# Kernel tuning notes

Hardware: AMD Instinct MI355X
Metric: run time of the kernel (lower is better)

The kernel has to match this reference:

```python
import math
import jax, jax.numpy as jnp
import numpy as np

N_HEAD = 16

def skew(QEr):
    # QEr: (B, H, L, L) where last dim indexes relative positions via Er_t
    B, H, L, _ = QEr.shape
    padded = jnp.pad(QEr, ((0, 0), (0, 0), (0, 0), (1, 0)))        # (B,H,L,L+1)
    reshaped = padded.reshape(B, H, L + 1, L)                       # (B,H,L+1,L)
    return reshaped[:, :, 1:, :]                                    # (B,H,L,L)

def setup_inputs() -> dict:
    key = jax.random.key(0)
    ks = jax.random.split(key, 6)
    B, L, D = 2, 2048, 1024
    hs = D // N_HEAD
    block_size = 2048
    return {
        "x": jax.random.normal(ks[0], (B, L, D), dtype=jnp.float32),
        "W_attn": jax.random.normal(ks[1], (D, 3 * D), dtype=jnp.float32) * 0.02,
        "b_attn": jnp.zeros((3 * D,), dtype=jnp.float32),
        "W_proj": jax.random.normal(ks[2], (D, D), dtype=jnp.float32) * 0.02,
        "b_proj": jnp.zeros((D,), dtype=jnp.float32),
        "Er": jax.random.normal(ks[3], (block_size, hs), dtype=jnp.float32),
    }

def reference(x, W_attn, b_attn, W_proj, b_proj, Er):
    B, L, D = x.shape
    H = N_HEAD
    hs = D // H
    qkv = x @ W_attn + b_attn                                       # (B,L,3D)
    q, k, v = jnp.split(qkv, 3, axis=-1)
    q = q.reshape(B, L, H, hs).transpose(0, 2, 1, 3)                # (B,H,L,hs)
    k = k.reshape(B, L, H, hs).transpose(0, 2, 1, 3)
    v = v.reshape(B, L, H, hs).transpose(0, 2, 1, 3)
    start = Er.shape[0] - L
    Er_t = Er[start:, :].T                                          # (hs,L)
    QEr = jnp.einsum('bhld,de->bhle', q, Er_t)                      # (B,H,L,L)
    Srel = skew(QEr)
    QK_t = jnp.einsum('bhqd,bhkd->bhqk', q, k)
    scale = 1.0 / math.sqrt(hs)
    att = (QK_t + Srel) * scale
    causal = jnp.tril(jnp.ones((L, L), dtype=bool))
    att = jnp.where(causal[None, None, :, :], att, -jnp.inf)
    att = jax.nn.softmax(att, axis=-1)
    y = jnp.einsum('bhqk,bhkd->bhqd', att, v)                       # (B,H,L,hs)
    y = y.transpose(0, 2, 1, 3).reshape(B, L, D)
    return y @ W_proj + b_proj
```

## Files before the change

### kernel.cpp

```cpp
#include <hip/hip_runtime.h>
#include <stdint.h>

#define L_SEQ 2048
#define D_MODEL 1024
#define NHEAD 16
#define HS 64
#define B_BATCH 2
#define QSCALE 0.1803368801111243f

typedef __bf16 bf16x8 __attribute__((ext_vector_type(8)));
typedef float f32x4 __attribute__((ext_vector_type(4)));

__device__ __forceinline__ float fexp2(float x) {
  return __builtin_amdgcn_exp2f(x);
}

__device__ __forceinline__ unsigned short f2b(float f) {
  unsigned int u = __float_as_uint(f);
  u += 0x7fffu + ((u >> 16) & 1u);
  return (unsigned short)(u >> 16);
}
__device__ __forceinline__ float b2f(unsigned short s) {
  return __uint_as_float(((unsigned int)s) << 16);
}
__device__ __forceinline__ unsigned int pk2(float a, float b) {
  return (unsigned int)f2b(a) | ((unsigned int)f2b(b) << 16);
}

union U8 { uint4 v; unsigned short s[8]; };

__device__ __forceinline__ void ldsload16(const unsigned short* g, unsigned short* l) {
  __builtin_amdgcn_global_load_lds(
      (const __attribute__((address_space(1))) unsigned int*)g,
      (__attribute__((address_space(3))) unsigned int*)l, 16, 0, 0);
}

__device__ __forceinline__ bf16x8 frag_ld(const unsigned short* base, int row, int ks, int quad) {
  const int unit = (ks * 4 + quad) ^ (row & 7);
  return *(const bf16x8*)(base + row * 64 + unit * 8);
}
__device__ __forceinline__ bf16x8 frag_ld88(const unsigned short* base, int row, int ks, int quad) {
  const int unit = (ks * 4 + quad) ^ (row & 7);
  return *(const bf16x8*)(base + row * 88 + unit * 8);
}

__global__ __launch_bounds__(256) void prep(
    const float* __restrict__ x, const float* __restrict__ Wa,
    const float* __restrict__ Wp, const float* __restrict__ Er,
    unsigned short* __restrict__ xb, unsigned short* __restrict__ wabT,
    unsigned short* __restrict__ wpbT, unsigned short* __restrict__ erb) {
  __shared__ unsigned short tt[64][65];
  int gb = blockIdx.x;
  if (gb < 2048) {
    int i = gb * 256 + threadIdx.x;
    const float4* s4 = (const float4*)x;
    float4 a = s4[i * 2], b = s4[i * 2 + 1];
    U8 u;
    u.s[0] = f2b(a.x); u.s[1] = f2b(a.y); u.s[2] = f2b(a.z); u.s[3] = f2b(a.w);
    u.s[4] = f2b(b.x); u.s[5] = f2b(b.y); u.s[6] = f2b(b.z); u.s[7] = f2b(b.w);
    ((uint4*)xb)[i] = u.v;
    return;
  }
  gb -= 2048;
  if (gb < 66) {
    int i = gb * 256 + threadIdx.x;
    if (i < 16384) {
      const float4* s4 = (const float4*)Er;
      float4 a = s4[i * 2], b = s4[i * 2 + 1];
      U8 u;
      u.s[0] = f2b(a.x); u.s[1] = f2b(a.y); u.s[2] = f2b(a.z); u.s[3] = f2b(a.w);
      u.s[4] = f2b(b.x); u.s[5] = f2b(b.y); u.s[6] = f2b(b.z); u.s[7] = f2b(b.w);
      ((uint4*)erb)[i] = u.v;
    } else {
      ((uint4*)erb)[i] = make_uint4(0u, 0u, 0u, 0u);
    }
    return;
  }
  gb -= 66;
  const float* src;
  unsigned short* dst;
  int N, nbx;
  if (gb < 768) { src = Wa; dst = wabT; N = 3072; nbx = 48; }
  else { gb -= 768; src = Wp; dst = wpbT; N = 1024; nbx = 16; }
  const int n0 = (gb % nbx) * 64, k0 = (gb / nbx) * 64;
  const int c = threadIdx.x & 63, r0 = threadIdx.x >> 6;
#pragma unroll
  for (int i = 0; i < 16; i++) {
    int r = r0 * 16 + i;
    tt[r][c] = f2b(src[(size_t)(k0 + r) * N + n0 + c]);
  }
  __syncthreads();
  const int n = threadIdx.x >> 2, ks = (threadIdx.x & 3) * 16;
  U8 u0, u1;
#pragma unroll
  for (int j = 0; j < 8; j++) {
    u0.s[j] = tt[ks + j][n];
    u1.s[j] = tt[ks + 8 + j][n];
  }
  unsigned short* d = dst + (size_t)(n0 + n) * 1024 + k0 + ks;
  *(uint4*)d = u0.v;
  *(uint4*)(d + 8) = u1.v;
}

__global__ __launch_bounds__(256, 3) void gemm_qkv(
    const unsigned short* __restrict__ A, const unsigned short* __restrict__ Bt,
    const float* __restrict__ bias, unsigned short* __restrict__ qbuf,
    unsigned short* __restrict__ kbuf, unsigned short* __restrict__ vbufT,
    int M, int N, int K) {
  __shared__ unsigned short SMEM[2 * 128 * 64];
  unsigned short* As = SMEM;
  unsigned short* Bs = SMEM + 128 * 64;
  const int tid = threadIdx.x, lane = tid & 63, w = tid >> 6;
  const int wm = w >> 1, wn = w & 1, quad = lane >> 4, lc = lane & 15;
  const int bm = blockIdx.y, bn = blockIdx.x;
  const int l8 = lane >> 3, u8 = ((lane & 7) ^ l8) * 8;
  const unsigned short* Ab = A + (size_t)bm * 128 * K;
  const unsigned short* Bb = Bt + (size_t)bn * 128 * K;

  f32x4 z4 = {0.f, 0.f, 0.f, 0.f};
  f32x4 acc[4][4];
#pragma unroll
  for (int mb = 0; mb < 4; mb++)
#pragma unroll
    for (int nb = 0; nb < 4; nb++) acc[mb][nb] = z4;

  for (int kk = 0; kk < K; kk += 64) {
    if (kk) __syncthreads();
#pragma unroll
    for (int i = 0; i < 4; i++) {
      int ch = w * 4 + i;
      ldsload16(Ab + (size_t)(ch * 8 + l8) * K + kk + u8, &As[ch * 512]);
      ldsload16(Bb + (size_t)(ch * 8 + l8) * K + kk + u8, &Bs[ch * 512]);
    }
    __syncthreads();
#pragma unroll
    for (int ks = 0; ks < 2; ks++) {
      bf16x8 af[4], bfv[4];
#pragma unroll
      for (int mb = 0; mb < 4; mb++) af[mb] = frag_ld(As, wm * 64 + mb * 16 + lc, ks, quad);
#pragma unroll
      for (int nb = 0; nb < 4; nb++) bfv[nb] = frag_ld(Bs, wn * 64 + nb * 16 + lc, ks, quad);
#pragma unroll
      for (int mb = 0; mb < 4; mb++)
#pragma unroll
        for (int nb = 0; nb < 4; nb++)
          acc[mb][nb] = __builtin_amdgcn_mfma_f32_16x16x32_bf16(af[mb], bfv[nb],
                                                               acc[mb][nb], 0, 0, 0);
    }
  }

  if (bn < 16) {
#pragma unroll
    for (int nb = 0; nb < 4; nb++) {
      const int n = bn * 128 + wn * 64 + nb * 16 + lc;
      const float bv = bias[n];
      const int which = n >> 10;
      const int rem = n & 1023;
      const int h = rem >> 6, d = rem & 63;
      unsigned short* dst = which == 0 ? qbuf : kbuf;
      const float sc = which == 0 ? QSCALE : 1.0f;
#pragma unroll
      for (int mb = 0; mb < 4; mb++) {
#pragma unroll
        for (int reg = 0; reg < 4; reg++) {
          const int m = bm * 128 + wm * 64 + mb * 16 + quad * 4 + reg;
          const int b = m >> 11, l = m & 2047;
          float val = (acc[mb][nb][reg] + bv) * sc;
          dst[((size_t)(b * NHEAD + h) * L_SEQ + l) * HS + d] = f2b(val);
        }
      }
    }
  } else {
    __syncthreads();
    unsigned short* Vs = SMEM;
#pragma unroll
    for (int nb = 0; nb < 4; nb++) {
      const int n_loc = wn * 64 + nb * 16 + lc;
      const float bv = bias[bn * 128 + n_loc];
#pragma unroll
      for (int mb = 0; mb < 4; mb++) {
#pragma unroll
        for (int reg = 0; reg < 4; reg++) {
          const int m_loc = wm * 64 + mb * 16 + quad * 4 + reg;
          Vs[n_loc * 128 + (((m_loc >> 3) ^ (n_loc & 15)) << 3) + (m_loc & 7)] =
              f2b(acc[mb][nb][reg] + bv);
        }
      }
    }
    __syncthreads();
    const int n_loc = tid >> 1, mh = tid & 1;
    const int n_glob = bn * 128 + n_loc;
    const int rem = n_glob & 1023;
    const int h = rem >> 6, d = rem & 63;
    const int b = bm >> 4;
    unsigned short* dstb =
        vbufT + ((size_t)(b * NHEAD + h) * HS + d) * L_SEQ + (bm & 15) * 128;
#pragma unroll
    for (int c = 0; c < 8; c++) {
      const int cg = mh * 8 + c;
      const int u = cg ^ (n_loc & 15);
      *(uint4*)(dstb + cg * 8) = *(const uint4*)&Vs[n_loc * 128 + u * 8];
    }
  }
}

__global__ __launch_bounds__(256, 2) void gemm_proj(
    const unsigned short* __restrict__ A, const unsigned short* __restrict__ Bt,
    const float* __restrict__ bias, float* __restrict__ out, int M, int N, int K) {
  __shared__ unsigned short As[128 * 64];
  __shared__ unsigned short Bs[64 * 64];
  const int tid = threadIdx.x, lane = tid & 63, w = tid >> 6;
  const int quad = lane >> 4, lc = lane & 15;
  const int bm = blockIdx.y, bn = blockIdx.x;
  const int l8 = lane >> 3, u8 = ((lane & 7) ^ l8) * 8;
  const unsigned short* Ab = A + (size_t)bm * 128 * K;
  const unsigned short* Bb = Bt + (size_t)bn * 64 * K;

  f32x4 z4 = {0.f, 0.f, 0.f, 0.f};
  f32x4 acc[2][4];
#pragma unroll
  for (int mb = 0; mb < 2; mb++)
#pragma unroll
    for (int nb = 0; nb < 4; nb++) acc[mb][nb] = z4;

  for (int kk = 0; kk < K; kk += 64) {
    if (kk) __syncthreads();
#pragma unroll
    for (int i = 0; i < 4; i++) {
      int ch = w * 4 + i;
      ldsload16(Ab + (size_t)(ch * 8 + l8) * K + kk + u8, &As[ch * 512]);
    }
#pragma unroll
    for (int i = 0; i < 2; i++) {
      int ch = w * 2 + i;
      ldsload16(Bb + (size_t)(ch * 8 + l8) * K + kk + u8, &Bs[ch * 512]);
    }
    __syncthreads();
#pragma unroll
    for (int ks = 0; ks < 2; ks++) {
      bf16x8 af[2], bfv[4];
#pragma unroll
      for (int mb = 0; mb < 2; mb++) af[mb] = frag_ld(As, w * 32 + mb * 16 + lc, ks, quad);
#pragma unroll
      for (int nb = 0; nb < 4; nb++) bfv[nb] = frag_ld(Bs, nb * 16 + lc, ks, quad);
#pragma unroll
      for (int mb = 0; mb < 2; mb++)
#pragma unroll
        for (int nb = 0; nb < 4; nb++)
          acc[mb][nb] = __builtin_amdgcn_mfma_f32_16x16x32_bf16(af[mb], bfv[nb],
                                                               acc[mb][nb], 0, 0, 0);
    }
  }

#pragma unroll
  for (int nb = 0; nb < 4; nb++) {
    const int n = bn * 64 + nb * 16 + lc;
    const float bv = bias[n];
#pragma unroll
    for (int mb = 0; mb < 2; mb++) {
#pragma unroll
      for (int reg = 0; reg < 4; reg++) {
        const int m = bm * 128 + w * 32 + mb * 16 + quad * 4 + reg;
        out[(size_t)m * N + n] = acc[mb][nb][reg] + bv;
      }
    }
  }
}

__global__ __launch_bounds__(256, 2) void flash_attn_rel(
    const unsigned short* __restrict__ qb, const unsigned short* __restrict__ kb,
    const unsigned short* __restrict__ vbT, const unsigned short* __restrict__ erb,
    unsigned short* __restrict__ yb) {
  __shared__ unsigned short Ks[2][64 * 64];
  __shared__ unsigned short Vt[2][64 * 64];
  __shared__ unsigned short Es[2][128 * 64];
  __shared__ unsigned short TP[4 * 16 * 88];

  const int tid = threadIdx.x, lane = tid & 63, w = tid >> 6;
  const int quad = lane >> 4, lc = lane & 15;
  const int bh = blockIdx.x;
  const int b = bh >> 4, h = bh & 15;
  const int j = blockIdx.y;
  const int qts0 = 31 - j, qts1 = j;
  const size_t hoff = (size_t)bh * L_SEQ * HS;
  unsigned short* TPw = TP + w * (16 * 88);
  const int l8 = lane >> 3, u8 = ((lane & 7) ^ l8) * 8;
  const f32x4 z4 = {0.f, 0.f, 0.f, 0.f};
  const unsigned short* kgb = kb + hoff;
  const unsigned short* vgbT = vbT + hoff;
  const int ebw = 48 - w * 16;

  auto stage = [&](int q0s, int k0s, int bufi) {
#pragma unroll
    for (int i = 0; i < 2; i++) {
      int ch = w * 2 + i;
      ldsload16(kgb + (size_t)(k0s + ch * 8 + l8) * HS + u8, &Ks[bufi][ch * 512]);
      ldsload16(vgbT + (size_t)(ch * 8 + l8) * L_SEQ + k0s + u8, &Vt[bufi][ch * 512]);
    }
    const int e0 = (L_SEQ - 64) - q0s + k0s;
#pragma unroll
    for (int i = 0; i < 4; i++) {
      int ch = w * 4 + i;
      ldsload16(erb + (size_t)(e0 + ch * 8 + l8) * HS + u8, &Es[bufi][ch * 512]);
    }
  };

  int buf = 0;
  stage(qts0 * 64, 0, 0);

#pragma unroll 1
  for (int phase = 0; phase < 2; phase++) {
    const int q0 = (phase == 0 ? qts0 : qts1) * 64;
    const int qg0 = q0 + w * 16;

    bf16x8 qf[2];
    {
      const unsigned short* qrow = qb + hoff + (size_t)(qg0 + lc) * HS;
      qf[0] = *(const bf16x8*)(qrow + quad * 8);
      qf[1] = *(const bf16x8*)(qrow + 32 + quad * 8);
    }
    f32x4 Oacc[4];
#pragma unroll
    for (int db = 0; db < 4; db++) Oacc[db] = z4;
    float psum_acc = 0.0f;

#pragma unroll 1
    for (int k0 = 0; k0 <= q0; k0 += 64) {
      __syncthreads();
      if (k0 + 64 <= q0) stage(q0, k0 + 64, buf ^ 1);
      else if (phase == 0) stage(qts1 * 64, 0, buf ^ 1);

      const unsigned short* KsB = Ks[buf];
      const unsigned short* VtB = Vt[buf];
      const unsigned short* EsB = Es[buf];

      f32x4 sacc[4], tacc[5];
#pragma unroll
      for (int i = 0; i < 4; i++) sacc[i] = z4;
#pragma unroll
      for (int i = 0; i < 5; i++) tacc[i] = z4;
#pragma unroll
      for (int ks = 0; ks < 2; ks++) {
#pragma unroll
        for (int kbi = 0; kbi < 4; kbi++) {
          bf16x8 a = frag_ld(KsB, kbi * 16 + lc, ks, quad);
          sacc[kbi] = __builtin_amdgcn_mfma_f32_16x16x32_bf16(a, qf[ks], sacc[kbi], 0, 0, 0);
        }
#pragma unroll
        for (int eb = 0; eb < 5; eb++) {
          bf16x8 a = frag_ld(EsB, ebw + eb * 16 + lc, ks, quad);
          tacc[eb] = __builtin_amdgcn_mfma_f32_16x16x32_bf16(a, qf[ks], tacc[eb], 0, 0, 0);
        }
      }
#pragma unroll
      for (int eb = 0; eb < 5; eb++) {
        uint2 pk;
        pk.x = pk2(tacc[eb][0], tacc[eb][1]);
        pk.y = pk2(tacc[eb][2], tacc[eb][3]);
        *(uint2*)&TPw[lc * 88 + eb * 16 + quad * 4] = pk;
      }
      asm volatile("" ::: "memory");

      float p[4][4], ps = 0.0f;
      const int tbase = lc * 88 + (15 - lc);
      if (k0 == q0) {
        const int qrow = w * 16 + lc;
#pragma unroll
        for (int kbi = 0; kbi < 4; kbi++)
#pragma unroll
          for (int reg = 0; reg < 4; reg++) {
            const int kk = kbi * 16 + quad * 4 + reg;
            float t = b2f(TPw[tbase + kk]);
            float v = (kk > qrow) ? -1e30f : (sacc[kbi][reg] + t);
            p[kbi][reg] = fexp2(v);
            ps += p[kbi][reg];
          }
      } else {
#pragma unroll
        for (int kbi = 0; kbi < 4; kbi++)
#pragma unroll
          for (int reg = 0; reg < 4; reg++) {
            float t = b2f(TPw[tbase + kbi * 16 + quad * 4 + reg]);
            p[kbi][reg] = fexp2(sacc[kbi][reg] + t);
            ps += p[kbi][reg];
          }
      }
      psum_acc += ps;
#pragma unroll
      for (int kbi = 0; kbi < 4; kbi++) {
        uint2 pk;
        pk.x = pk2(p[kbi][0], p[kbi][1]);
        pk.y = pk2(p[kbi][2], p[kbi][3]);
        const int kk2 = kbi * 16 + quad * 4;
        *(uint2*)&TPw[lc * 88 + (((kk2 >> 3) ^ (lc & 7)) << 3) + (kk2 & 7)] = pk;
      }
      asm volatile("" ::: "memory");

#pragma unroll
      for (int ks = 0; ks < 2; ks++) {
        bf16x8 pf = frag_ld88(TPw, lc, ks, quad);
#pragma unroll
        for (int db = 0; db < 4; db++) {
          bf16x8 av = frag_ld(VtB, db * 16 + lc, ks, quad);
          Oacc[db] = __builtin_amdgcn_mfma_f32_16x16x32_bf16(av, pf, Oacc[db], 0, 0, 0);
        }
      }
      buf ^= 1;
    }

    psum_acc += __shfl_xor(psum_acc, 16, 64);
    psum_acc += __shfl_xor(psum_acc, 32, 64);
    const float inv = 1.0f / psum_acc;
    __syncthreads();
    unsigned short* Yt = TP;
#pragma unroll
    for (int db = 0; db < 4; db++) {
      uint2 pk;
      pk.x = pk2(Oacc[db][0] * inv, Oacc[db][1] * inv);
      pk.y = pk2(Oacc[db][2] * inv, Oacc[db][3] * inv);
      *(uint2*)&Yt[(w * 16 + lc) * 72 + db * 16 + quad * 4] = pk;
    }
    __syncthreads();
    {
      const int r = tid >> 2, seg = (tid & 3) * 16;
      uint4 a0 = *(const uint4*)&Yt[r * 72 + seg];
      uint4 a1 = *(const uint4*)&Yt[r * 72 + seg + 8];
      unsigned short* d = yb + (size_t)((size_t)b * L_SEQ + q0 + r) * D_MODEL + h * HS + seg;
      *(uint4*)d = a0;
      *(uint4*)(d + 8) = a1;
    }
  }
}

extern "C" void kernel_launch(void* const* d_in, const int* in_sizes, int n_in,
                              void* d_out, int out_size, void* d_ws, size_t ws_size,
                              hipStream_t stream) {
  const float* x = (const float*)d_in[0];
  const float* W_attn = (const float*)d_in[1];
  const float* b_attn = (const float*)d_in[2];
  const float* W_proj = (const float*)d_in[3];
  const float* b_proj = (const float*)d_in[4];
  const float* Er = (const float*)d_in[5];
  float* out = (float*)d_out;

  const int n_x = B_BATCH * L_SEQ * D_MODEL;
  const int n_wa = D_MODEL * 3 * D_MODEL;
  const int n_wp = D_MODEL * D_MODEL;
  const int n_er_pad = (L_SEQ + 64) * HS;
  const int n_head = B_BATCH * NHEAD * L_SEQ * HS;

  unsigned short* xb = (unsigned short*)d_ws;
  unsigned short* wabT = xb + n_x;
  unsigned short* wpbT = wabT + n_wa;
  unsigned short* erb = wpbT + n_wp;
  unsigned short* qbuf = erb + n_er_pad;
  unsigned short* kbuf = qbuf + n_head;
  unsigned short* vbufT = kbuf + n_head;
  unsigned short* ybuf = vbufT + n_head;

  prep<<<3138, 256, 0, stream>>>(x, W_attn, W_proj, Er, xb, wabT, wpbT, erb);

  gemm_qkv<<<dim3(24, 32), 256, 0, stream>>>(xb, wabT, b_attn, qbuf, kbuf, vbufT,
                                             B_BATCH * L_SEQ, 3 * D_MODEL, D_MODEL);

  flash_attn_rel<<<dim3(B_BATCH * NHEAD, 16), 256, 0, stream>>>(qbuf, kbuf, vbufT,
                                                                erb, ybuf);

  gemm_proj<<<dim3(16, 32), 256, 0, stream>>>(ybuf, wpbT, b_proj, out,
                                              B_BATCH * L_SEQ, D_MODEL, D_MODEL);
}
```

Measured before the change: 228.8 us.

## Process adjacent query tiles together to share K/V/Er tiles, drop double buffering

Each attention block now handles two adjacent 64-row query tiles at once instead of a mirrored pair processed one after the other. Each loaded K, V and a widened 192-row Er tile is reused by both tiles, which halves the K/V staging per unit of work. The LDS double buffering is removed and occupancy is raised to 3 blocks per SM. In exchange, global loads are no longer overlapped with compute, the load balance across blocks is worse than with the mirrored pairing, and the Er padding buffer grows to cover the extra rows.

```diff
diff --git a/kernel.cpp b/kernel.cpp
--- a/kernel.cpp
+++ b/kernel.cpp
@@ -62,7 +62,7 @@
     return;
   }
   gb -= 2048;
-  if (gb < 66) {
+  if (gb < 68) {
     int i = gb * 256 + threadIdx.x;
     if (i < 16384) {
       const float4* s4 = (const float4*)Er;
@@ -71,12 +71,12 @@
       u.s[0] = f2b(a.x); u.s[1] = f2b(a.y); u.s[2] = f2b(a.z); u.s[3] = f2b(a.w);
       u.s[4] = f2b(b.x); u.s[5] = f2b(b.y); u.s[6] = f2b(b.z); u.s[7] = f2b(b.w);
       ((uint4*)erb)[i] = u.v;
-    } else {
+    } else if (i < 17408) {
       ((uint4*)erb)[i] = make_uint4(0u, 0u, 0u, 0u);
     }
     return;
   }
-  gb -= 66;
+  gb -= 68;
   const float* src;
   unsigned short* dst;
   int N, nbx;
@@ -267,168 +267,192 @@
   }
 }
 
-__global__ __launch_bounds__(256, 2) void flash_attn_rel(
+__global__ __launch_bounds__(256, 3) void flash_attn_rel(
     const unsigned short* __restrict__ qb, const unsigned short* __restrict__ kb,
     const unsigned short* __restrict__ vbT, const unsigned short* __restrict__ erb,
     unsigned short* __restrict__ yb) {
-  __shared__ unsigned short Ks[2][64 * 64];
-  __shared__ unsigned short Vt[2][64 * 64];
-  __shared__ unsigned short Es[2][128 * 64];
+  __shared__ unsigned short Ks[64 * 64];
+  __shared__ unsigned short Vt[64 * 64];
+  __shared__ unsigned short Es[192 * 64];
   __shared__ unsigned short TP[4 * 16 * 88];
 
   const int tid = threadIdx.x, lane = tid & 63, w = tid >> 6;
   const int quad = lane >> 4, lc = lane & 15;
   const int bh = blockIdx.x;
   const int b = bh >> 4, h = bh & 15;
-  const int j = blockIdx.y;
-  const int qts0 = 31 - j, qts1 = j;
+  const int p = 15 - (int)blockIdx.y;
+  const int q0lo = 2 * p * 64, q0hi = q0lo + 64;
   const size_t hoff = (size_t)bh * L_SEQ * HS;
   unsigned short* TPw = TP + w * (16 * 88);
   const int l8 = lane >> 3, u8 = ((lane & 7) ^ l8) * 8;
   const f32x4 z4 = {0.f, 0.f, 0.f, 0.f};
   const unsigned short* kgb = kb + hoff;
   const unsigned short* vgbT = vbT + hoff;
-  const int ebw = 48 - w * 16;
-
-  auto stage = [&](int q0s, int k0s, int bufi) {
+
+  bf16x8 qfh[2], qfl[2];
+  {
+    const unsigned short* qh = qb + hoff + (size_t)(q0hi + w * 16 + lc) * HS;
+    const unsigned short* ql = qb + hoff + (size_t)(q0lo + w * 16 + lc) * HS;
+    qfh[0] = *(const bf16x8*)(qh + quad * 8);
+    qfh[1] = *(const bf16x8*)(qh + 32 + quad * 8);
+    qfl[0] = *(const bf16x8*)(ql + quad * 8);
+    qfl[1] = *(const bf16x8*)(ql + 32 + quad * 8);
+  }
+  f32x4 Oh[4], Ol[4];
+#pragma unroll
+  for (int db = 0; db < 4; db++) { Oh[db] = z4; Ol[db] = z4; }
+  float psh = 0.0f, psl = 0.0f;
+
+  auto softmax_pv = [&](f32x4 (&sacc)[4], f32x4 (&tacc)[5], bool diag,
+                        float& psum_acc, f32x4 (&Oacc)[4], bf16x8 (&vf)[2][4]) {
+#pragma unroll
+    for (int eb = 0; eb < 5; eb++) {
+      uint2 pk;
+      pk.x = pk2(tacc[eb][0], tacc[eb][1]);
+      pk.y = pk2(tacc[eb][2], tacc[eb][3]);
+      *(uint2*)&TPw[lc * 88 + eb * 16 + quad * 4] = pk;
+    }
+    asm volatile("" ::: "memory");
+    float pv[4][4], ps = 0.0f;
+    const int tbase = lc * 88 + (15 - lc);
+    if (diag) {
+      const int qrow = w * 16 + lc;
+#pragma unroll
+      for (int kbi = 0; kbi < 4; kbi++)
+#pragma unroll
+        for (int reg = 0; reg < 4; reg++) {
+          const int kk = kbi * 16 + quad * 4 + reg;
+          float t = b2f(TPw[tbase + kk]);
+          float v = (kk > qrow) ? -1e30f : (sacc[kbi][reg] + t);
+          pv[kbi][reg] = fexp2(v);
+          ps += pv[kbi][reg];
+        }
+    } else {
+#pragma unroll
+      for (int kbi = 0; kbi < 4; kbi++)
+#pragma unroll
+        for (int reg = 0; reg < 4; reg++) {
+          float t = b2f(TPw[tbase + kbi * 16 + quad * 4 + reg]);
+          pv[kbi][reg] = fexp2(sacc[kbi][reg] + t);
+          ps += pv[kbi][reg];
+        }
+    }
+    psum_acc += ps;
+#pragma unroll
+    for (int kbi = 0; kbi < 4; kbi++) {
+      uint2 pk;
+      pk.x = pk2(pv[kbi][0], pv[kbi][1]);
+      pk.y = pk2(pv[kbi][2], pv[kbi][3]);
+      const int kk2 = kbi * 16 + quad * 4;
+      *(uint2*)&TPw[lc * 88 + (((kk2 >> 3) ^ (lc & 7)) << 3) + (kk2 & 7)] = pk;
+    }
+    asm volatile("" ::: "memory");
+#pragma unroll
+    for (int ks = 0; ks < 2; ks++) {
+      bf16x8 pf = frag_ld88(TPw, lc, ks, quad);
+#pragma unroll
+      for (int db = 0; db < 4; db++)
+        Oacc[db] = __builtin_amdgcn_mfma_f32_16x16x32_bf16(vf[ks][db], pf, Oacc[db], 0, 0, 0);
+    }
+  };
+
+#pragma unroll 1
+  for (int k0 = 0; k0 <= q0hi; k0 += 64) {
+    const bool lo_active = (k0 <= q0lo);
+    __syncthreads();
 #pragma unroll
     for (int i = 0; i < 2; i++) {
       int ch = w * 2 + i;
-      ldsload16(kgb + (size_t)(k0s + ch * 8 + l8) * HS + u8, &Ks[bufi][ch * 512]);
-      ldsload16(vgbT + (size_t)(ch * 8 + l8) * L_SEQ + k0s + u8, &Vt[bufi][ch * 512]);
-    }
-    const int e0 = (L_SEQ - 64) - q0s + k0s;
-#pragma unroll
-    for (int i = 0; i < 4; i++) {
-      int ch = w * 4 + i;
-      ldsload16(erb + (size_t)(e0 + ch * 8 + l8) * HS + u8, &Es[bufi][ch * 512]);
-    }
-  };
-
-  int buf = 0;
-  stage(qts0 * 64, 0, 0);
-
+      ldsload16(kgb + (size_t)(k0 + ch * 8 + l8) * HS + u8, &Ks[ch * 512]);
+      ldsload16(vgbT + (size_t)(ch * 8 + l8) * L_SEQ + k0 + u8, &Vt[ch * 512]);
+    }
+    const int e0 = (L_SEQ - 64) - q0hi + k0;
+#pragma unroll
+    for (int i = 0; i < 6; i++) {
+      int ch = w * 6 + i;
+      ldsload16(erb + (size_t)(e0 + ch * 8 + l8) * HS + u8, &Es[ch * 512]);
+    }
+    __syncthreads();
+
+    f32x4 sh[4], sl[4];
+#pragma unroll
+    for (int i = 0; i < 4; i++) { sh[i] = z4; sl[i] = z4; }
+#pragma unroll
+    for (int ks = 0; ks < 2; ks++) {
+      bf16x8 kf[4];
+#pragma unroll
+      for (int kbi = 0; kbi < 4; kbi++) kf[kbi] = frag_ld(Ks, kbi * 16 + lc, ks, quad);
+#pragma unroll
+      for (int kbi = 0; kbi < 4; kbi++)
+        sh[kbi] = __builtin_amdgcn_mfma_f32_16x16x32_bf16(kf[kbi], qfh[ks], sh[kbi], 0, 0, 0);
+      if (lo_active) {
+#pragma unroll
+        for (int kbi = 0; kbi < 4; kbi++)
+          sl[kbi] = __builtin_amdgcn_mfma_f32_16x16x32_bf16(kf[kbi], qfl[ks], sl[kbi], 0, 0, 0);
+      }
+    }
+
+    f32x4 th[5];
+#pragma unroll
+    for (int i = 0; i < 5; i++) th[i] = z4;
+    const int rsh = 48 - w * 16;
+#pragma unroll
+    for (int ks = 0; ks < 2; ks++)
+#pragma unroll
+      for (int eb = 0; eb < 5; eb++)
+        th[eb] = __builtin_amdgcn_mfma_f32_16x16x32_bf16(
+            frag_ld(Es, rsh + eb * 16 + lc, ks, quad), qfh[ks], th[eb], 0, 0, 0);
+
+    bf16x8 vf[2][4];
+#pragma unroll
+    for (int ks = 0; ks < 2; ks++)
+#pragma unroll
+      for (int db = 0; db < 4; db++) vf[ks][db] = frag_ld(Vt, db * 16 + lc, ks, quad);
+
+    softmax_pv(sh, th, k0 == q0hi, psh, Oh, vf);
+
+    if (lo_active) {
+      f32x4 tl[5];
+#pragma unroll
+      for (int i = 0; i < 5; i++) tl[i] = z4;
+      const int rsl = 112 - w * 16;
+#pragma unroll
+      for (int ks = 0; ks < 2; ks++)
+#pragma unroll
+        for (int eb = 0; eb < 5; eb++)
+          tl[eb] = __builtin_amdgcn_mfma_f32_16x16x32_bf16(
+              frag_ld(Es, rsl + eb * 16 + lc, ks, quad), qfl[ks], tl[eb], 0, 0, 0);
+      softmax_pv(sl, tl, k0 == q0lo, psl, Ol, vf);
+    }
+  }
+
+  psh += __shfl_xor(psh, 16, 64);
+  psh += __shfl_xor(psh, 32, 64);
+  psl += __shfl_xor(psl, 16, 64);
+  psl += __shfl_xor(psl, 32, 64);
+  const float invh = 1.0f / psh, invl = 1.0f / psl;
+
+  unsigned short* Yt = TP;
 #pragma unroll 1
-  for (int phase = 0; phase < 2; phase++) {
-    const int q0 = (phase == 0 ? qts0 : qts1) * 64;
-    const int qg0 = q0 + w * 16;
-
-    bf16x8 qf[2];
-    {
-      const unsigned short* qrow = qb + hoff + (size_t)(qg0 + lc) * HS;
-      qf[0] = *(const bf16x8*)(qrow + quad * 8);
-      qf[1] = *(const bf16x8*)(qrow + 32 + quad * 8);
-    }
-    f32x4 Oacc[4];
-#pragma unroll
-    for (int db = 0; db < 4; db++) Oacc[db] = z4;
-    float psum_acc = 0.0f;
-
-#pragma unroll 1
-    for (int k0 = 0; k0 <= q0; k0 += 64) {
-      __syncthreads();
-      if (k0 + 64 <= q0) stage(q0, k0 + 64, buf ^ 1);
-      else if (phase == 0) stage(qts1 * 64, 0, buf ^ 1);
-
-      const unsigned short* KsB = Ks[buf];
-      const unsigned short* VtB = Vt[buf];
-      const unsigned short* EsB = Es[buf];
-
-      f32x4 sacc[4], tacc[5];
-#pragma unroll
-      for (int i = 0; i < 4; i++) sacc[i] = z4;
-#pragma unroll
-      for (int i = 0; i < 5; i++) tacc[i] = z4;
-#pragma unroll
-      for (int ks = 0; ks < 2; ks++) {
-#pragma unroll
-        for (int kbi = 0; kbi < 4; kbi++) {
-          bf16x8 a = frag_ld(KsB, kbi * 16 + lc, ks, quad);
-          sacc[kbi] = __builtin_amdgcn_mfma_f32_16x16x32_bf16(a, qf[ks], sacc[kbi], 0, 0, 0);
-        }
-#pragma unroll
-        for (int eb = 0; eb < 5; eb++) {
-          bf16x8 a = frag_ld(EsB, ebw + eb * 16 + lc, ks, quad);
-          tacc[eb] = __builtin_amdgcn_mfma_f32_16x16x32_bf16(a, qf[ks], tacc[eb], 0, 0, 0);
-        }
-      }
-#pragma unroll
-      for (int eb = 0; eb < 5; eb++) {
-        uint2 pk;
-        pk.x = pk2(tacc[eb][0], tacc[eb][1]);
-        pk.y = pk2(tacc[eb][2], tacc[eb][3]);
-        *(uint2*)&TPw[lc * 88 + eb * 16 + quad * 4] = pk;
-      }
-      asm volatile("" ::: "memory");
-
-      float p[4][4], ps = 0.0f;
-      const int tbase = lc * 88 + (15 - lc);
-      if (k0 == q0) {
-        const int qrow = w * 16 + lc;
-#pragma unroll
-        for (int kbi = 0; kbi < 4; kbi++)
-#pragma unroll
-          for (int reg = 0; reg < 4; reg++) {
-            const int kk = kbi * 16 + quad * 4 + reg;
-            float t = b2f(TPw[tbase + kk]);
-            float v = (kk > qrow) ? -1e30f : (sacc[kbi][reg] + t);
-            p[kbi][reg] = fexp2(v);
-            ps += p[kbi][reg];
-          }
-      } else {
-#pragma unroll
-        for (int kbi = 0; kbi < 4; kbi++)
-#pragma unroll
-          for (int reg = 0; reg < 4; reg++) {
-            float t = b2f(TPw[tbase + kbi * 16 + quad * 4 + reg]);
-            p[kbi][reg] = fexp2(sacc[kbi][reg] + t);
-            ps += p[kbi][reg];
-          }
-      }
-      psum_acc += ps;
-#pragma unroll
-      for (int kbi = 0; kbi < 4; kbi++) {
-        uint2 pk;
-        pk.x = pk2(p[kbi][0], p[kbi][1]);
-        pk.y = pk2(p[kbi][2], p[kbi][3]);
-        const int kk2 = kbi * 16 + quad * 4;
-        *(uint2*)&TPw[lc * 88 + (((kk2 >> 3) ^ (lc & 7)) << 3) + (kk2 & 7)] = pk;
-      }
-      asm volatile("" ::: "memory");
-
-#pragma unroll
-      for (int ks = 0; ks < 2; ks++) {
-        bf16x8 pf = frag_ld88(TPw, lc, ks, quad);
-#pragma unroll
-        for (int db = 0; db < 4; db++) {
-          bf16x8 av = frag_ld(VtB, db * 16 + lc, ks, quad);
-          Oacc[db] = __builtin_amdgcn_mfma_f32_16x16x32_bf16(av, pf, Oacc[db], 0, 0, 0);
-        }
-      }
-      buf ^= 1;
-    }
-
-    psum_acc += __shfl_xor(psum_acc, 16, 64);
-    psum_acc += __shfl_xor(psum_acc, 32, 64);
-    const float inv = 1.0f / psum_acc;
-    __syncthreads();
-    unsigned short* Yt = TP;
+  for (int t = 0; t < 2; t++) {
+    const float inv = t == 0 ? invh : invl;
+    const int q0 = t == 0 ? q0hi : q0lo;
+    f32x4* O = t == 0 ? Oh : Ol;
+    __syncthreads();
 #pragma unroll
     for (int db = 0; db < 4; db++) {
       uint2 pk;
-      pk.x = pk2(Oacc[db][0] * inv, Oacc[db][1] * inv);
-      pk.y = pk2(Oacc[db][2] * inv, Oacc[db][3] * inv);
+      pk.x = pk2(O[db][0] * inv, O[db][1] * inv);
+      pk.y = pk2(O[db][2] * inv, O[db][3] * inv);
       *(uint2*)&Yt[(w * 16 + lc) * 72 + db * 16 + quad * 4] = pk;
     }
     __syncthreads();
-    {
-      const int r = tid >> 2, seg = (tid & 3) * 16;
-      uint4 a0 = *(const uint4*)&Yt[r * 72 + seg];
-      uint4 a1 = *(const uint4*)&Yt[r * 72 + seg + 8];
-      unsigned short* d = yb + (size_t)((size_t)b * L_SEQ + q0 + r) * D_MODEL + h * HS + seg;
-      *(uint4*)d = a0;
-      *(uint4*)(d + 8) = a1;
-    }
+    const int r = tid >> 2, seg = (tid & 3) * 16;
+    uint4 a0 = *(const uint4*)&Yt[r * 72 + seg];
+    uint4 a1 = *(const uint4*)&Yt[r * 72 + seg + 8];
+    unsigned short* d = yb + (size_t)((size_t)b * L_SEQ + q0 + r) * D_MODEL + h * HS + seg;
+    *(uint4*)d = a0;
+    *(uint4*)(d + 8) = a1;
   }
 }
 
@@ -446,7 +470,7 @@
   const int n_x = B_BATCH * L_SEQ * D_MODEL;
   const int n_wa = D_MODEL * 3 * D_MODEL;
   const int n_wp = D_MODEL * D_MODEL;
-  const int n_er_pad = (L_SEQ + 64) * HS;
+  const int n_er_pad = (L_SEQ + 128) * HS;
   const int n_head = B_BATCH * NHEAD * L_SEQ * HS;
 
   unsigned short* xb = (unsigned short*)d_ws;
@@ -458,7 +482,7 @@
   unsigned short* vbufT = kbuf + n_head;
   unsigned short* ybuf = vbufT + n_head;
 
-  prep<<<3138, 256, 0, stream>>>(x, W_attn, W_proj, Er, xb, wabT, wpbT, erb);
+  prep<<<3140, 256, 0, stream>>>(x, W_attn, W_proj, Er, xb, wabT, wpbT, erb);
 
   gemm_qkv<<<dim3(24, 32), 256, 0, stream>>>(xb, wabT, b_attn, qbuf, kbuf, vbufT,
                                              B_BATCH * L_SEQ, 3 * D_MODEL, D_MODEL);
```

New measurement: 270.1 us. 1.18x slower.

## Use one query tile per block with register-staged K/Er and direct V loads

Applied to the files above, without the earlier changes.

Removes the paired-tile (31-j, j) scheme so each block handles a single query tile, doubling the grid. The double-buffered LDS async staging is replaced by register prefetch of the next K and Er tiles followed by explicit LDS stores. V fragments are now read straight from global memory instead of LDS. Together these shrink LDS usage and raise the launch bounds to 4 blocks per CU for more occupancy. The costs are an extra sync per iteration, uneven per-block work from the causal mask, and uncoalesced global V reads.

```diff
diff --git a/kernel.cpp b/kernel.cpp
--- a/kernel.cpp
+++ b/kernel.cpp
@@ -267,21 +267,21 @@
   }
 }
 
-__global__ __launch_bounds__(256, 2) void flash_attn_rel(
+__global__ __launch_bounds__(256, 4) void flash_attn_rel(
     const unsigned short* __restrict__ qb, const unsigned short* __restrict__ kb,
     const unsigned short* __restrict__ vbT, const unsigned short* __restrict__ erb,
     unsigned short* __restrict__ yb) {
-  __shared__ unsigned short Ks[2][64 * 64];
-  __shared__ unsigned short Vt[2][64 * 64];
-  __shared__ unsigned short Es[2][128 * 64];
+  __shared__ unsigned short Ks[64 * 64];
+  __shared__ unsigned short Es[128 * 64];
   __shared__ unsigned short TP[4 * 16 * 88];
 
   const int tid = threadIdx.x, lane = tid & 63, w = tid >> 6;
   const int quad = lane >> 4, lc = lane & 15;
   const int bh = blockIdx.x;
   const int b = bh >> 4, h = bh & 15;
-  const int j = blockIdx.y;
-  const int qts0 = 31 - j, qts1 = j;
+  const int qt = 31 - (int)blockIdx.y;
+  const int q0 = qt * 64;
+  const int qg0 = q0 + w * 16;
   const size_t hoff = (size_t)bh * L_SEQ * HS;
   unsigned short* TPw = TP + w * (16 * 88);
   const int l8 = lane >> 3, u8 = ((lane & 7) ^ l8) * 8;
@@ -290,145 +290,151 @@
   const unsigned short* vgbT = vbT + hoff;
   const int ebw = 48 - w * 16;
 
-  auto stage = [&](int q0s, int k0s, int bufi) {
-#pragma unroll
-    for (int i = 0; i < 2; i++) {
-      int ch = w * 2 + i;
-      ldsload16(kgb + (size_t)(k0s + ch * 8 + l8) * HS + u8, &Ks[bufi][ch * 512]);
-      ldsload16(vgbT + (size_t)(ch * 8 + l8) * L_SEQ + k0s + u8, &Vt[bufi][ch * 512]);
-    }
-    const int e0 = (L_SEQ - 64) - q0s + k0s;
-#pragma unroll
-    for (int i = 0; i < 4; i++) {
-      int ch = w * 4 + i;
-      ldsload16(erb + (size_t)(e0 + ch * 8 + l8) * HS + u8, &Es[bufi][ch * 512]);
-    }
-  };
-
-  int buf = 0;
-  stage(qts0 * 64, 0, 0);
+  bf16x8 qf[2];
+  {
+    const unsigned short* qrow = qb + hoff + (size_t)(qg0 + lc) * HS;
+    qf[0] = *(const bf16x8*)(qrow + quad * 8);
+    qf[1] = *(const bf16x8*)(qrow + 32 + quad * 8);
+  }
+  f32x4 Oacc[4];
+#pragma unroll
+  for (int db = 0; db < 4; db++) Oacc[db] = z4;
+  float psum_acc = 0.0f;
+
+  const unsigned short* kga[2];
+  const unsigned short* ega[4];
+#pragma unroll
+  for (int i = 0; i < 2; i++) kga[i] = kgb + (size_t)((w * 2 + i) * 8 + l8) * HS + u8;
+#pragma unroll
+  for (int i = 0; i < 4; i++) ega[i] = erb + (size_t)((w * 4 + i) * 8 + l8) * HS + u8;
+  const int e00 = (L_SEQ - 64) - q0;
+
+  uint4 kr[2], er[4];
+#pragma unroll
+  for (int i = 0; i < 2; i++) kr[i] = *(const uint4*)(kga[i]);
+#pragma unroll
+  for (int i = 0; i < 4; i++) er[i] = *(const uint4*)(ega[i] + (size_t)e00 * HS);
 
 #pragma unroll 1
-  for (int phase = 0; phase < 2; phase++) {
-    const int q0 = (phase == 0 ? qts0 : qts1) * 64;
-    const int qg0 = q0 + w * 16;
-
-    bf16x8 qf[2];
-    {
-      const unsigned short* qrow = qb + hoff + (size_t)(qg0 + lc) * HS;
-      qf[0] = *(const bf16x8*)(qrow + quad * 8);
-      qf[1] = *(const bf16x8*)(qrow + 32 + quad * 8);
-    }
-    f32x4 Oacc[4];
-#pragma unroll
-    for (int db = 0; db < 4; db++) Oacc[db] = z4;
-    float psum_acc = 0.0f;
-
-#pragma unroll 1
-    for (int k0 = 0; k0 <= q0; k0 += 64) {
-      __syncthreads();
-      if (k0 + 64 <= q0) stage(q0, k0 + 64, buf ^ 1);
-      else if (phase == 0) stage(qts1 * 64, 0, buf ^ 1);
-
-      const unsigned short* KsB = Ks[buf];
-      const unsigned short* VtB = Vt[buf];
-      const unsigned short* EsB = Es[buf];
-
-      f32x4 sacc[4], tacc[5];
-#pragma unroll
-      for (int i = 0; i < 4; i++) sacc[i] = z4;
-#pragma unroll
-      for (int i = 0; i < 5; i++) tacc[i] = z4;
-#pragma unroll
-      for (int ks = 0; ks < 2; ks++) {
-#pragma unroll
-        for (int kbi = 0; kbi < 4; kbi++) {
-          bf16x8 a = frag_ld(KsB, kbi * 16 + lc, ks, quad);
-          sacc[kbi] = __builtin_amdgcn_mfma_f32_16x16x32_bf16(a, qf[ks], sacc[kbi], 0, 0, 0);
+  for (int k0 = 0; k0 <= q0; k0 += 64) {
+    __syncthreads();
+#pragma unroll
+    for (int i = 0; i < 2; i++)
+      *(uint4*)&Ks[(w * 2 + i) * 512 + lane * 8] = kr[i];
+#pragma unroll
+    for (int i = 0; i < 4; i++)
+      *(uint4*)&Es[(w * 4 + i) * 512 + lane * 8] = er[i];
+    __syncthreads();
+
+    if (k0 + 64 <= q0) {
+      const int kn = k0 + 64;
+#pragma unroll
+      for (int i = 0; i < 2; i++) kr[i] = *(const uint4*)(kga[i] + (size_t)kn * HS);
+#pragma unroll
+      for (int i = 0; i < 4; i++)
+        er[i] = *(const uint4*)(ega[i] + (size_t)(e00 + kn) * HS);
+    }
+
+    f32x4 sacc[4], tacc[5];
+#pragma unroll
+    for (int i = 0; i < 4; i++) sacc[i] = z4;
+#pragma unroll
+    for (int i = 0; i < 5; i++) tacc[i] = z4;
+#pragma unroll
+    for (int ks = 0; ks < 2; ks++) {
+#pragma unroll
+      for (int kbi = 0; kbi < 4; kbi++) {
+        bf16x8 a = frag_ld(Ks, kbi * 16 + lc, ks, quad);
+        sacc[kbi] = __builtin_amdgcn_mfma_f32_16x16x32_bf16(a, qf[ks], sacc[kbi], 0, 0, 0);
+      }
+#pragma unroll
+      for (int eb = 0; eb < 5; eb++) {
+        bf16x8 a = frag_ld(Es, ebw + eb * 16 + lc, ks, quad);
+        tacc[eb] = __builtin_amdgcn_mfma_f32_16x16x32_bf16(a, qf[ks], tacc[eb], 0, 0, 0);
+      }
+    }
+#pragma unroll
+    for (int eb = 0; eb < 5; eb++) {
+      uint2 pk;
+      pk.x = pk2(tacc[eb][0], tacc[eb][1]);
+      pk.y = pk2(tacc[eb][2], tacc[eb][3]);
+      *(uint2*)&TPw[lc * 88 + eb * 16 + quad * 4] = pk;
+    }
+    asm volatile("" ::: "memory");
+
+    bf16x8 vf[2][4];
+#pragma unroll
+    for (int ks = 0; ks < 2; ks++)
+#pragma unroll
+      for (int db = 0; db < 4; db++)
+        vf[ks][db] = *(const bf16x8*)(vgbT + (size_t)(db * 16 + lc) * L_SEQ + k0 +
+                                      ks * 32 + quad * 8);
+
+    float p[4][4], ps = 0.0f;
+    const int tbase = lc * 88 + (15 - lc);
+    if (k0 == q0) {
+      const int qrow = w * 16 + lc;
+#pragma unroll
+      for (int kbi = 0; kbi < 4; kbi++)
+#pragma unroll
+        for (int reg = 0; reg < 4; reg++) {
+          const int kk = kbi * 16 + quad * 4 + reg;
+          float t = b2f(TPw[tbase + kk]);
+          float v = (kk > qrow) ? -1e30f : (sacc[kbi][reg] + t);
+          p[kbi][reg] = fexp2(v);
+          ps += p[kbi][reg];
         }
-#pragma unroll
-        for (int eb = 0; eb < 5; eb++) {
-          bf16x8 a = frag_ld(EsB, ebw + eb * 16 + lc, ks, quad);
-          tacc[eb] = __builtin_amdgcn_mfma_f32_16x16x32_bf16(a, qf[ks], tacc[eb], 0, 0, 0);
+    } else {
+#pragma unroll
+      for (int kbi = 0; kbi < 4; kbi++)
+#pragma unroll
+        for (int reg = 0; reg < 4; reg++) {
+          float t = b2f(TPw[tbase + kbi * 16 + quad * 4 + reg]);
+          p[kbi][reg] = fexp2(sacc[kbi][reg] + t);
+          ps += p[kbi][reg];
         }
-      }
-#pragma unroll
-      for (int eb = 0; eb < 5; eb++) {
-        uint2 pk;
-        pk.x = pk2(tacc[eb][0], tacc[eb][1]);
-        pk.y = pk2(tacc[eb][2], tacc[eb][3]);
-        *(uint2*)&TPw[lc * 88 + eb * 16 + quad * 4] = pk;
-      }
-      asm volatile("" ::: "memory");
-
-      float p[4][4], ps = 0.0f;
-      const int tbase = lc * 88 + (15 - lc);
-      if (k0 == q0) {
-        const int qrow = w * 16 + lc;
-#pragma unroll
-        for (int kbi = 0; kbi < 4; kbi++)
-#pragma unroll
-          for (int reg = 0; reg < 4; reg++) {
-            const int kk = kbi * 16 + quad * 4 + reg;
-            float t = b2f(TPw[tbase + kk]);
-            float v = (kk > qrow) ? -1e30f : (sacc[kbi][reg] + t);
-            p[kbi][reg] = fexp2(v);
-            ps += p[kbi][reg];
-          }
-      } else {
-#pragma unroll
-        for (int kbi = 0; kbi < 4; kbi++)
-#pragma unroll
-          for (int reg = 0; reg < 4; reg++) {
-            float t = b2f(TPw[tbase + kbi * 16 + quad * 4 + reg]);
-            p[kbi][reg] = fexp2(sacc[kbi][reg] + t);
-            ps += p[kbi][reg];
-          }
-      }
-      psum_acc += ps;
-#pragma unroll
-      for (int kbi = 0; kbi < 4; kbi++) {
-        uint2 pk;
-        pk.x = pk2(p[kbi][0], p[kbi][1]);
-        pk.y = pk2(p[kbi][2], p[kbi][3]);
-        const int kk2 = kbi * 16 + quad * 4;
-        *(uint2*)&TPw[lc * 88 + (((kk2 >> 3) ^ (lc & 7)) << 3) + (kk2 & 7)] = pk;
-      }
-      asm volatile("" ::: "memory");
-
-#pragma unroll
-      for (int ks = 0; ks < 2; ks++) {
-        bf16x8 pf = frag_ld88(TPw, lc, ks, quad);
-#pragma unroll
-        for (int db = 0; db < 4; db++) {
-          bf16x8 av = frag_ld(VtB, db * 16 + lc, ks, quad);
-          Oacc[db] = __builtin_amdgcn_mfma_f32_16x16x32_bf16(av, pf, Oacc[db], 0, 0, 0);
-        }
-      }
-      buf ^= 1;
-    }
-
-    psum_acc += __shfl_xor(psum_acc, 16, 64);
-    psum_acc += __shfl_xor(psum_acc, 32, 64);
-    const float inv = 1.0f / psum_acc;
-    __syncthreads();
-    unsigned short* Yt = TP;
-#pragma unroll
-    for (int db = 0; db < 4; db++) {
+    }
+    psum_acc += ps;
+#pragma unroll
+    for (int kbi = 0; kbi < 4; kbi++) {
       uint2 pk;
-      pk.x = pk2(Oacc[db][0] * inv, Oacc[db][1] * inv);
-      pk.y = pk2(Oacc[db][2] * inv, Oacc[db][3] * inv);
-      *(uint2*)&Yt[(w * 16 + lc) * 72 + db * 16 + quad * 4] = pk;
-    }
-    __syncthreads();
-    {
-      const int r = tid >> 2, seg = (tid & 3) * 16;
-      uint4 a0 = *(const uint4*)&Yt[r * 72 + seg];
-      uint4 a1 = *(const uint4*)&Yt[r * 72 + seg + 8];
-      unsigned short* d = yb + (size_t)((size_t)b * L_SEQ + q0 + r) * D_MODEL + h * HS + seg;
-      *(uint4*)d = a0;
-      *(uint4*)(d + 8) = a1;
-    }
+      pk.x = pk2(p[kbi][0], p[kbi][1]);
+      pk.y = pk2(p[kbi][2], p[kbi][3]);
+      const int kk2 = kbi * 16 + quad * 4;
+      *(uint2*)&TPw[lc * 88 + (((kk2 >> 3) ^ (lc & 7)) << 3) + (kk2 & 7)] = pk;
+    }
+    asm volatile("" ::: "memory");
+
+#pragma unroll
+    for (int ks = 0; ks < 2; ks++) {
+      bf16x8 pf = frag_ld88(TPw, lc, ks, quad);
+#pragma unroll
+      for (int db = 0; db < 4; db++)
+        Oacc[db] = __builtin_amdgcn_mfma_f32_16x16x32_bf16(vf[ks][db], pf, Oacc[db], 0, 0, 0);
+    }
+  }
+
+  psum_acc += __shfl_xor(psum_acc, 16, 64);
+  psum_acc += __shfl_xor(psum_acc, 32, 64);
+  const float inv = 1.0f / psum_acc;
+
+  __syncthreads();
+  unsigned short* Yt = TP;
+#pragma unroll
+  for (int db = 0; db < 4; db++) {
+    uint2 pk;
+    pk.x = pk2(Oacc[db][0] * inv, Oacc[db][1] * inv);
+    pk.y = pk2(Oacc[db][2] * inv, Oacc[db][3] * inv);
+    *(uint2*)&Yt[(w * 16 + lc) * 72 + db * 16 + quad * 4] = pk;
+  }
+  __syncthreads();
+  {
+    const int r = tid >> 2, seg = (tid & 3) * 16;
+    uint4 a0 = *(const uint4*)&Yt[r * 72 + seg];
+    uint4 a1 = *(const uint4*)&Yt[r * 72 + seg + 8];
+    unsigned short* d = yb + (size_t)((size_t)b * L_SEQ + q0 + r) * D_MODEL + h * HS + seg;
+    *(uint4*)d = a0;
+    *(uint4*)(d + 8) = a1;
   }
 }
 
@@ -463,7 +469,7 @@
   gemm_qkv<<<dim3(24, 32), 256, 0, stream>>>(xb, wabT, b_attn, qbuf, kbuf, vbufT,
                                              B_BATCH * L_SEQ, 3 * D_MODEL, D_MODEL);
 
-  flash_attn_rel<<<dim3(B_BATCH * NHEAD, 16), 256, 0, stream>>>(qbuf, kbuf, vbufT,
+  flash_attn_rel<<<dim3(B_BATCH * NHEAD, 32), 256, 0, stream>>>(qbuf, kbuf, vbufT,
                                                                 erb, ybuf);
 
   gemm_proj<<<dim3(16, 32), 256, 0, stream>>>(ybuf, wpbT, b_proj, out,
```

After: 320.5 us. 40.1% more time.
